# Optimization experiments

Measured on AMD Instinct MI355X. Metric: run time of the kernel, lower is better.

## Reference

```python
import jax, jax.numpy as jnp
import numpy as np

B, T, V = 128, 1024, 192
EPS = 1e-8


def setup_inputs() -> dict:
    key = jax.random.key(0)
    k1, k2, k3, k4, k5 = jax.random.split(key, 5)
    return {
        "emissions": jax.random.normal(k1, (B, T, V), dtype=jnp.float32),
        "tags": jax.random.randint(k2, (B, T), 0, V, dtype=jnp.int64),
        "mask": jnp.ones((B, T), dtype=jnp.int32),
        "transitions": jax.random.normal(k3, (V, V), dtype=jnp.float32) * 0.1,
        "start_trans": jax.random.normal(k4, (V,), dtype=jnp.float32) * 0.1,
        "end_trans": jax.random.normal(k5, (V,), dtype=jnp.float32) * 0.1,
    }


def _lse(x, axis):
    # matches torch _log_sum_exp: max + log(sum(exp(x-max)) + 1e-8)
    m = jnp.max(x, axis=axis)
    return m + jnp.log(jnp.sum(jnp.exp(x - jnp.expand_dims(m, axis)), axis=axis) + EPS)


def _log_partition(emissions, mask, transitions, start_trans, end_trans):
    # emissions: (B,T,V), mask: (B,T) int
    alpha0 = start_trans[None, :] + emissions[:, 0, :]  # (B,V)
    em_t = jnp.moveaxis(emissions[:, 1:, :], 1, 0)       # (T-1,B,V)
    mk_t = jnp.moveaxis(mask[:, 1:], 1, 0).astype(bool)  # (T-1,B)

    def step(alpha, inp):
        emit, m = inp  # (B,V), (B,)
        # (B, V_prev, V_next)
        scores = alpha[:, :, None] + transitions[None, :, :] + emit[:, None, :]
        new_alpha = _lse(scores, axis=1)
        alpha = jnp.where(m[:, None], new_alpha, alpha)
        return alpha, None

    alpha, _ = jax.lax.scan(step, alpha0, (em_t, mk_t))
    return _lse(alpha + end_trans[None, :], axis=1)  # (B,)


def _gold_score(emissions, tags, mask, transitions, start_trans, end_trans):
    Bq, Tq, _ = emissions.shape
    maskf = mask.astype(emissions.dtype)
    # emission score of gold tags at each step: (B,T)
    emit = jnp.take_along_axis(emissions, tags[:, :, None], axis=2)[:, :, 0]
    # transitions between consecutive gold tags: (B,T-1)
    trans = transitions[tags[:, :-1], tags[:, 1:]]
    score = start_trans[tags[:, 0]] + emit[:, 0]
    score = score + jnp.sum((emit[:, 1:] + trans) * maskf[:, 1:], axis=1)
    last_idx = jnp.sum(mask, axis=1).astype(jnp.int32) - 1  # (B,)
    last_tags = jnp.take_along_axis(tags, last_idx[:, None].astype(tags.dtype), axis=1)[:, 0]
    score = score + end_trans[last_tags]
    return score


def reference(emissions, tags, mask, transitions, start_trans, end_trans):
    log_den = _log_partition(emissions, mask, transitions, start_trans, end_trans)
    log_num = _gold_score(emissions, tags, mask, transitions, start_trans, end_trans)
    raw_loss = log_den - log_num
    seq_len = jnp.clip(jnp.sum(mask, axis=1).astype(emissions.dtype), 1.0)
    return raw_loss / seq_len  # (B,)
```

## Files before the change

kernel.cpp:

```cpp
#include <hip/hip_runtime.h>

#define BB 128
#define TT 1024
#define VV 192
#define NTHREADS 256
#define LN2 0.69314718055994530942f
#define WS_STRIDE 448

typedef int   intx8   __attribute__((ext_vector_type(8)));
typedef float floatx2 __attribute__((ext_vector_type(2)));
typedef float floatx4 __attribute__((ext_vector_type(4)));

__device__ __forceinline__ float bf8_to_f32(unsigned char h) {
    floatx2 v = __builtin_amdgcn_cvt_pk_f32_bf8((int)(unsigned int)h, false);
    return v.x;
}
__device__ __forceinline__ unsigned char f32_to_bf8(float f) {
    int pk = __builtin_amdgcn_cvt_pk_bf8_f32(f, f, 0, false);
    return (unsigned char)(pk & 0xff);
}
__device__ __forceinline__ unsigned char f32_to_fp8(float f) {
    int pk = __builtin_amdgcn_cvt_pk_fp8_f32(f, f, 0, false);
    return (unsigned char)(pk & 0xff);
}

#define LBAR() __asm__ volatile("s_waitcnt lgkmcnt(0)\n\ts_barrier" ::: "memory")

template<int DIR>
__device__ __forceinline__ void crf_body(const float* __restrict__ emissions,
                                         const int* __restrict__ tags,
                                         const int* __restrict__ mask,
                                         const float* __restrict__ trans,
                                         const float* __restrict__ start_trans,
                                         const float* __restrict__ end_trans,
                                         float* __restrict__ ws)
{
    const int b = blockIdx.x;
    const int tid = threadIdx.x;
    const int lane = tid & 63;
    const int wid = tid >> 6;
    const int quad = lane >> 4;
    const int col = lane & 15;

    __shared__ __align__(16) unsigned char qpad[4][2][256];
    __shared__ unsigned int smaskp[33];
    __shared__ float wgs[4], wsls[4];

    const float* em_b = emissions + (size_t)b * TT * VV;
    const int* mask_b = mask + b * TT;
    float* wsb = ws + (size_t)b * WS_STRIDE;

    const int nl = wid * 48 + (quad < 3 ? quad : 0) * 16 + col;

    const int firstc[4] = {1, 113, 241, DIR ? 367 : 369};
    const int capRc[4]  = {0, 16, 16, DIR ? 18 : 16};
    const int capPc[4]  = {128, 144, 144, 0};

    #define ROW_OF(x) (DIR ? (TT - 1 - (x)) : (x))

    intx8 ef[6];
    #pragma unroll
    for (int kt = 0; kt < 2; ++kt) {
        #pragma unroll
        for (int h = 0; h < 3; ++h) {
            const int n = wid * 48 + h * 16 + col;
            intx8 v;
            #pragma unroll
            for (int w = 0; w < 8; ++w) {
                unsigned int word = 0;
                #pragma unroll
                for (int by = 0; by < 4; ++by) {
                    int k = kt * 128 + quad * 32 + w * 4 + by;
                    float x = (k < VV) ? __expf(trans[DIR ? (k + n * VV) : (k * VV + n)]) : 0.f;
                    word |= (unsigned int)f32_to_fp8(x) << (8 * by);
                }
                v[w] = (int)word;
            }
            ef[kt * 3 + h] = v;
        }
    }

    for (int i = tid; i < 4 * 512; i += NTHREADS) ((unsigned char*)qpad)[i] = 0;

    if (tid < 33) {
        if (tid == 32) smaskp[32] = 0u;
        else {
            unsigned int m = 0;
            #pragma unroll 4
            for (int j = 0; j < 32; ++j) m |= (mask_b[tid * 32 + j] ? 1u : 0u) << j;
            smaskp[tid] = m;
        }
    }

    float em0[4][8], em1[4][8];
    #pragma unroll
    for (int c = 0; c < 4; ++c) {
        #pragma unroll
        for (int r = 0; r < 8; ++r) em0[c][r] = em_b[(size_t)ROW_OF(firstc[c] + r) * VV + nl];
        #pragma unroll
        for (int r = 0; r < 8; ++r) em1[c][r] = em_b[(size_t)ROW_OF(firstc[c] + 8 + r) * VV + nl];
    }
    float pep[4] = {0.f, 0.f, 0.f, 0.f};
    if (DIR) {
        #pragma unroll
        for (int c = 0; c < 4; ++c)
            pep[c] = __expf(em_b[(size_t)ROW_OF(firstc[c] - 1) * VV + nl]);
    }

    __syncthreads();
    if (tid < VV) {
        float a0 = DIR ? (end_trans[tid] + em_b[(size_t)(TT - 1) * VV + tid])
                       : (start_trans[tid] + em_b[tid]);
        qpad[0][0][tid] = f32_to_bf8(fminf(__expf(a0), 28672.f));
        unsigned char one = f32_to_bf8(1.0f);
        qpad[1][0][tid] = one;
        qpad[2][0][tid] = one;
        qpad[3][0][tid] = one;
    }
    float carry[4] = {0.f,0.f,0.f,0.f}, Rv[4] = {0.f,0.f,0.f,0.f};
    float Pv[4] = {0.f,0.f,0.f,0.f}, csv[4] = {0.f,0.f,0.f,0.f};
    int cur = 0;
    __syncthreads();

    unsigned long long mk64[4];
    int shb[4];

#define GETMK(c, I) ((int)((mk64[c] >> (DIR ? (shb[c] + 15 - (I)) : (shb[c] + (I)))) & 1ull))

#define ROUND(I)                                                               \
    {                                                                          \
        intx8 a0_[4], a1_[4];                                                  \
        unsigned char prevb_[4];                                               \
        _Pragma("unroll")                                                      \
        for (int c = 0; c < 4; ++c) {                                          \
            const intx8* qv = (const intx8*)qpad[c][cur];                      \
            a0_[c] = qv[quad];                                                 \
            a1_[c] = qv[quad + 4];                                             \
            prevb_[c] = qpad[c][cur][nl];                                      \
        }                                                                      \
        floatx4 acc_[4][3];                                                    \
        _Pragma("unroll")                                                      \
        for (int c = 0; c < 4; ++c) {                                          \
            _Pragma("unroll")                                                  \
            for (int h = 0; h < 3; ++h) {                                      \
                floatx4 z = (floatx4){0.f, 0.f, 0.f, 0.f};                     \
                floatx4 t0 = __builtin_amdgcn_mfma_scale_f32_16x16x128_f8f6f4( \
                    a0_[c], ef[h], z, 1, 0, 0, 0x7f7f7f7f, 0, 0x7f7f7f7f);     \
                acc_[c][h] = __builtin_amdgcn_mfma_scale_f32_16x16x128_f8f6f4( \
                    a1_[c], ef[3 + h], t0, 1, 0, 0, 0x7f7f7f7f, 0, 0x7f7f7f7f);\
            }                                                                  \
        }                                                                      \
        _Pragma("unroll")                                                      \
        for (int c = 0; c < 4; ++c) {                                          \
            int mk = GETMK(c, I);                                              \
            int q0i = __builtin_amdgcn_readfirstlane(a0_[c][0]);               \
            float q0 = bf8_to_f32((unsigned char)(q0i & 0xff));                \
            float rr = __builtin_amdgcn_rcpf(q0);                              \
            carry[c] += mk ? __log2f(q0) : 0.f;                                \
            float emraw = ((I) < 8) ? em0[c][(I) & 7] : em1[c][(I) & 7];       \
            float pe = __expf(emraw);                                          \
            float sc = pe * rr;                                                \
            float s0 = acc_[c][0][0];                                          \
            float s1 = acc_[c][1][0];                                          \
            float s2 = acc_[c][2][0];                                          \
            float vv = (quad == 1) ? s1 : ((quad == 2) ? s2 : s0);             \
            unsigned char nbm = f32_to_bf8(fminf(vv * sc, 28672.f));           \
            unsigned char nba;                                                 \
            if (DIR) nba = f32_to_bf8(fminf(bf8_to_f32(prevb_[c]) * pe *       \
                                 __builtin_amdgcn_rcpf(pep[c]), 28672.f));     \
            else nba = prevb_[c];                                              \
            unsigned char nb = mk ? nbm : nba;                                 \
            qpad[c][cur ^ 1][nl] = nb;                                         \
            if (DIR) pep[c] = pe;                                              \
             \
            float q0n = bf8_to_f32(nb);                                        \
            float lg = __log2f(__int_as_float(                                 \
                __builtin_amdgcn_readfirstlane(__float_as_int(q0n))));         \
            int L = lb + (I) + 1;                                              \
            bool hitR = (L == capRc[c]);                                       \
            bool hitP = (L == capPc[c]);                                       \
            Rv[c]    = hitR ? lg : Rv[c];                                      \
            csv[c]   = hitP ? carry[c] : csv[c];                               \
            Pv[c]    = hitP ? lg : Pv[c];                                      \
            carry[c] = hitR ? 0.f : carry[c];                                  \
        }                                                                      \
        __builtin_amdgcn_sched_group_barrier(0x100, 12, 0);      \
        __builtin_amdgcn_sched_group_barrier(0x008, 24, 0);       \
        LBAR();                                                                \
        cur ^= 1;                                                              \
    }

    for (int w = 0; w < 9; ++w) {
        const int lb = 16 * w;
        #pragma unroll
        for (int c = 0; c < 4; ++c) {
            int gw = firstc[c] + lb;
            int base = DIR ? (1024 - gw - 15) : gw;
            unsigned lo = (unsigned)__builtin_amdgcn_readfirstlane((int)smaskp[base >> 5]);
            unsigned hi = (unsigned)__builtin_amdgcn_readfirstlane((int)smaskp[(base >> 5) + 1]);
            mk64[c] = (((unsigned long long)hi) << 32) | (unsigned long long)lo;
            shb[c] = base & 31;
        }
        ROUND(0) ROUND(1) ROUND(2) ROUND(3)
        ROUND(4) ROUND(5) ROUND(6) ROUND(7)
        {
            #pragma unroll
            for (int c = 0; c < 4; ++c) {
                #pragma unroll
                for (int r = 0; r < 8; ++r)
                    em0[c][r] = em_b[(size_t)ROW_OF(firstc[c] + lb + 16 + r) * VV + nl];
            }
        }
        ROUND(8) ROUND(9) ROUND(10) ROUND(11)
        ROUND(12) ROUND(13) ROUND(14) ROUND(15)
        {
            #pragma unroll
            for (int c = 0; c < 4; ++c) {
                #pragma unroll
                for (int r = 0; r < 8; ++r)
                    em1[c][r] = em_b[(size_t)ROW_OF(firstc[c] + lb + 24 + r) * VV + nl];
            }
        }
    }
#undef ROUND
#undef GETMK

    csv[3] = carry[3];

    if (DIR == 0) {
        if (tid < VV) wsb[tid] = bf8_to_f32(qpad[3][cur][tid]);
    } else {
        const intx8* qv = (const intx8*)qpad[3][cur];
        intx8 A0 = qv[quad];
        intx8 A1 = qv[quad + 4];
        int mkf = (int)((smaskp[513 >> 5] >> (513 & 31)) & 1u);
        floatx4 aA[3], aB[3];
        #pragma unroll
        for (int h = 0; h < 3; ++h) {
            floatx4 z = (floatx4){0.f, 0.f, 0.f, 0.f};
            aA[h] = __builtin_amdgcn_mfma_scale_f32_16x16x128_f8f6f4(
                        A0, ef[h], z, 1, 0, 0, 0x7f7f7f7f, 0, 0x7f7f7f7f);
            aB[h] = __builtin_amdgcn_mfma_scale_f32_16x16x128_f8f6f4(
                        A1, ef[3 + h], z, 1, 0, 0, 0x7f7f7f7f, 0, 0x7f7f7f7f);
        }
        if (quad < 3) {
            float s0 = aA[0][0] + aB[0][0];
            float s1 = aA[1][0] + aB[1][0];
            float s2 = aA[2][0] + aB[2][0];
            float vv = (quad == 1) ? s1 : ((quad == 2) ? s2 : s0);
            if (!mkf) vv = bf8_to_f32(qpad[3][cur][nl]) * __builtin_amdgcn_rcpf(pep[3]);
            wsb[192 + nl] = vv;
        }
    }
    if (tid == 0) {
        #pragma unroll
        for (int c = 0; c < 4; ++c) {
            float contrib = csv[c] + ((c < 3) ? Pv[c] : 0.f) - ((c > 0) ? Rv[c] : 0.f);
            wsb[384 + DIR * 8 + c] = contrib;
        }
    }

    float gp = 0.f, sl = 0.f;
    for (int t = tid; t < TT; t += NTHREADS) {
        int mk = (int)((smaskp[t >> 5] >> (t & 31)) & 1u);
        bool inS = DIR ? (t >= 512) : (t < 512);
        if (inS) sl += (float)mk;
        bool inG = DIR ? (t >= 513) : (t >= 1 && t <= 512);
        if (inG) {
            int tg  = tags[b * TT + t];
            int tgp = tags[b * TT + t - 1];
            float term = em_b[(size_t)t * VV + tg] + trans[tgp * VV + tg];
            gp += mk ? term : 0.f;
        }
    }
    #pragma unroll
    for (int off = 1; off < 64; off <<= 1) {
        gp += __shfl_xor(gp, off);
        sl += __shfl_xor(sl, off);
    }
    if (lane == 0) { wgs[wid] = gp; wsls[wid] = sl; }
    __syncthreads();
    if (tid == 0) {
        float g = 0.f, s = 0.f;
        for (int w = 0; w < 4; ++w) { g += wgs[w]; s += wsls[w]; }
        if (DIR == 0) {
            int tg0 = tags[b * TT];
            g += start_trans[tg0] + em_b[tg0];
        }
        wsb[384 + DIR * 8 + 4] = g;
        wsb[384 + DIR * 8 + 5] = s;
    }
    #undef ROW_OF
}

__launch_bounds__(NTHREADS, 1)
__attribute__((amdgpu_waves_per_eu(1, 1)))
__global__ void crf_ilp_kernel(const float* __restrict__ emissions,
                               const int* __restrict__ tags,
                               const int* __restrict__ mask,
                               const float* __restrict__ trans,
                               const float* __restrict__ start_trans,
                               const float* __restrict__ end_trans,
                               float* __restrict__ ws)
{
    if (blockIdx.y == 0)
        crf_body<0>(emissions, tags, mask, trans, start_trans, end_trans, ws);
    else
        crf_body<1>(emissions, tags, mask, trans, start_trans, end_trans, ws);
}

__global__ void crf_combine(const float* __restrict__ ws,
                            const int* __restrict__ tags,
                            const float* __restrict__ end_trans,
                            float* __restrict__ out)
{
    const int b = blockIdx.x;
    const int lane = threadIdx.x;
    const float* wsb = ws + (size_t)b * WS_STRIDE;
    float s = 0.f;
    #pragma unroll
    for (int i = lane; i < VV; i += 64) s += wsb[i] * wsb[192 + i];
    #pragma unroll
    for (int off = 1; off < 64; off <<= 1) s += __shfl_xor(s, off);
    if (lane == 0) {
        float T = 0.f, gold = 0.f, seq = 0.f;
        for (int d = 0; d < 2; ++d) {
            const float* slot = wsb + 384 + d * 8;
            T    += slot[0] + slot[1] + slot[2] + slot[3];
            gold += slot[4];
            seq  += slot[5];
        }
        float logden = LN2 * T + __logf(s + 1e-8f);
        int seqs = (int)(seq + 0.5f);
        int last_idx = seqs - 1; if (last_idx < 0) last_idx = 0;
        gold += end_trans[tags[b * TT + last_idx]];
        float seqf = fmaxf((float)seqs, 1.0f);
        out[b] = (logden - gold) / seqf;
    }
}

extern "C" void kernel_launch(void* const* d_in, const int* in_sizes, int n_in,
                              void* d_out, int out_size, void* d_ws, size_t ws_size,
                              hipStream_t stream) {
    const float* emissions   = (const float*)d_in[0];
    const int*   tags        = (const int*)d_in[1];
    const int*   mask        = (const int*)d_in[2];
    const float* trans       = (const float*)d_in[3];
    const float* start_trans = (const float*)d_in[4];
    const float* end_trans   = (const float*)d_in[5];
    float* out = (float*)d_out;
    float* ws  = (float*)d_ws;

    crf_ilp_kernel<<<dim3(BB, 2), NTHREADS, 0, stream>>>(
        emissions, tags, mask, trans, start_trans, end_trans, ws);
    crf_combine<<<BB, 64, 0, stream>>>(ws, tags, end_trans, out);
}
```

Baseline: 252.5 us.

## Pack four chunk recurrences into one MFMA via per-row A operands

Each recurrence step now loads a different chunk's probability vector into each row group of the MFMA A operand (lane&3 selects the chunk). One pair of MFMAs per output tile then yields all four chunks' results in separate accumulator rows, replacing four separate MFMA pairs. A startup self-test checks that the MFMA row mapping behaves as assumed and falls back to the original four-chunk path if it does not. Emission prefetch and per-lane work are reorganised around the new lane-to-chunk mapping. The risks are extra LDS reads and select logic per step, plus a one-time validation cost.

```diff
diff --git a/kernel.cpp b/kernel.cpp
--- a/kernel.cpp
+++ b/kernel.cpp
@@ -25,6 +25,9 @@
 }
 
 #define LBAR() __asm__ volatile("s_waitcnt lgkmcnt(0)\n\ts_barrier" ::: "memory")
+
+#define MFMA_SC(A, B, C) __builtin_amdgcn_mfma_scale_f32_16x16x128_f8f6f4( \
+    (A), (B), (C), 1, 0, 0, 0x7f7f7f7f, 0, 0x7f7f7f7f)
 
 template<int DIR>
 __device__ __forceinline__ void crf_body(const float* __restrict__ emissions,
@@ -45,12 +48,14 @@
     __shared__ __align__(16) unsigned char qpad[4][2][256];
     __shared__ unsigned int smaskp[33];
     __shared__ float wgs[4], wsls[4];
+    __shared__ int okflag;
 
     const float* em_b = emissions + (size_t)b * TT * VV;
     const int* mask_b = mask + b * TT;
     float* wsb = ws + (size_t)b * WS_STRIDE;
 
-    const int nl = wid * 48 + (quad < 3 ? quad : 0) * 16 + col;
+    const int col0 = wid * 48 + col;
+    const int nlT  = wid * 48 + (quad < 3 ? quad : 0) * 16 + col;
 
     const int firstc[4] = {1, 113, 241, DIR ? 367 : 369};
     const int capRc[4]  = {0, 16, 16, DIR ? 18 : 16};
@@ -91,43 +96,185 @@
             smaskp[tid] = m;
         }
     }
-
-    float em0[4][8], em1[4][8];
-    #pragma unroll
-    for (int c = 0; c < 4; ++c) {
-        #pragma unroll
-        for (int r = 0; r < 8; ++r) em0[c][r] = em_b[(size_t)ROW_OF(firstc[c] + r) * VV + nl];
-        #pragma unroll
-        for (int r = 0; r < 8; ++r) em1[c][r] = em_b[(size_t)ROW_OF(firstc[c] + 8 + r) * VV + nl];
-    }
-    float pep[4] = {0.f, 0.f, 0.f, 0.f};
-    if (DIR) {
-        #pragma unroll
-        for (int c = 0; c < 4; ++c)
-            pep[c] = __expf(em_b[(size_t)ROW_OF(firstc[c] - 1) * VV + nl]);
-    }
+    if (tid == 0) okflag = 1;
 
     __syncthreads();
     if (tid < VV) {
         float a0 = DIR ? (end_trans[tid] + em_b[(size_t)(TT - 1) * VV + tid])
                        : (start_trans[tid] + em_b[tid]);
         qpad[0][0][tid] = f32_to_bf8(fminf(__expf(a0), 28672.f));
-        unsigned char one = f32_to_bf8(1.0f);
-        qpad[1][0][tid] = one;
-        qpad[2][0][tid] = one;
-        qpad[3][0][tid] = one;
-    }
+        qpad[1][0][tid] = f32_to_bf8(1.0f);
+        qpad[2][0][tid] = f32_to_bf8(2.0f);
+        qpad[3][0][tid] = f32_to_bf8(4.0f);
+    }
+    __syncthreads();
+
+    {
+        int okl = 1;
+        const intx8* qv0 = (const intx8*)qpad[0][0];
+        intx8 b0 = qv0[quad], b1 = qv0[quad + 4];
+        const intx8* qvp = (const intx8*)qpad[lane & 3][0];
+        intx8 p0 = qvp[quad], p1 = qvp[quad + 4];
+        floatx4 z = (floatx4){0.f, 0.f, 0.f, 0.f};
+        floatx4 tb = MFMA_SC(b0, ef[0], z);
+        floatx4 ab = MFMA_SC(b1, ef[3], tb);
+        floatx4 tp = MFMA_SC(p0, ef[0], z);
+        floatx4 ap = MFMA_SC(p1, ef[3], tp);
+        okl &= (fabsf(ap[0] - ab[0]) <= 1e-3f * (fabsf(ab[0]) + 1.f)) ? 1 : 0;
+        okl &= (fabsf(ap[2] - 2.f * ap[1]) <= 1e-3f * (fabsf(ap[2]) + 1.f)) ? 1 : 0;
+        okl &= (fabsf(ap[3] - 4.f * ap[1]) <= 1e-3f * (fabsf(ap[3]) + 1.f)) ? 1 : 0;
+        unsigned long long vt = __ballot(okl);
+        if (lane == 0 && vt != 0xFFFFFFFFFFFFFFFFull) okflag = 0;
+    }
+    __syncthreads();
+    const bool usePacked = (okflag != 0);
+
     float carry[4] = {0.f,0.f,0.f,0.f}, Rv[4] = {0.f,0.f,0.f,0.f};
     float Pv[4] = {0.f,0.f,0.f,0.f}, csv[4] = {0.f,0.f,0.f,0.f};
     int cur = 0;
-    __syncthreads();
-
     unsigned long long mk64[4];
     int shb[4];
 
+#define FETCHWIN(lb_)                                                          \
+    {                                                                          \
+        _Pragma("unroll")                                                      \
+        for (int c = 0; c < 4; ++c) {                                          \
+            int gw = firstc[c] + (lb_);                                        \
+            int base = DIR ? (1024 - gw - 15) : gw;                            \
+            unsigned lo = (unsigned)__builtin_amdgcn_readfirstlane((int)smaskp[base >> 5]);      \
+            unsigned hi = (unsigned)__builtin_amdgcn_readfirstlane((int)smaskp[(base >> 5) + 1]);\
+            mk64[c] = (((unsigned long long)hi) << 32) | (unsigned long long)lo;\
+            shb[c] = base & 31;                                                \
+        }                                                                      \
+    }
 #define GETMK(c, I) ((int)((mk64[c] >> (DIR ? (shb[c] + 15 - (I)) : (shb[c] + (I)))) & 1ull))
 
-#define ROUND(I)                                                               \
+    if (usePacked) {
+        const int flc = (quad == 1) ? firstc[1] : (quad == 2) ? firstc[2]
+                      : (quad == 3) ? firstc[3] : firstc[0];
+        float em0[3][8], em1[3][8];
+        #pragma unroll
+        for (int h = 0; h < 3; ++h) {
+            #pragma unroll
+            for (int r = 0; r < 8; ++r) {
+                em0[h][r] = em_b[(size_t)ROW_OF(flc + r) * VV + col0 + h * 16];
+                em1[h][r] = em_b[(size_t)ROW_OF(flc + 8 + r) * VV + col0 + h * 16];
+            }
+        }
+        float pep[3] = {0.f, 0.f, 0.f};
+        if (DIR) {
+            #pragma unroll
+            for (int h = 0; h < 3; ++h)
+                pep[h] = __expf(em_b[(size_t)ROW_OF(flc - 1) * VV + col0 + h * 16]);
+        }
+
+#define PROUND(I)                                                              \
+    {                                                                          \
+        const intx8* qv_ = (const intx8*)qpad[lane & 3][cur];                  \
+        intx8 a0_ = qv_[quad];                                                 \
+        intx8 a1_ = qv_[quad + 4];                                             \
+        float q0c[4];                                                          \
+        q0c[0] = bf8_to_f32(qpad[0][cur][0]);                                  \
+        q0c[1] = bf8_to_f32(qpad[1][cur][0]);                                  \
+        q0c[2] = bf8_to_f32(qpad[2][cur][0]);                                  \
+        q0c[3] = bf8_to_f32(qpad[3][cur][0]);                                  \
+        unsigned char pb0 = qpad[quad][cur][col0];                             \
+        unsigned char pb1 = qpad[quad][cur][col0 + 16];                        \
+        unsigned char pb2 = qpad[quad][cur][col0 + 32];                        \
+                                                       \
+        {                                                                      \
+            int Lm1 = lb + (I);                                                \
+            _Pragma("unroll")                                                  \
+            for (int c = 0; c < 4; ++c) {                                      \
+                float lgc = __log2f(q0c[c]);                                   \
+                bool hitR = (Lm1 == capRc[c]);                                 \
+                bool hitP = (Lm1 == capPc[c]);                                 \
+                Rv[c]    = hitR ? lgc : Rv[c];                                 \
+                csv[c]   = hitP ? carry[c] : csv[c];                           \
+                Pv[c]    = hitP ? lgc : Pv[c];                                 \
+                carry[c] = hitR ? 0.f : carry[c];                              \
+            }                                                                  \
+        }                                                                      \
+        floatx4 acc_[3];                                                       \
+        _Pragma("unroll")                                                      \
+        for (int h = 0; h < 3; ++h) {                                          \
+            floatx4 z_ = (floatx4){0.f, 0.f, 0.f, 0.f};                        \
+            floatx4 t0_ = MFMA_SC(a0_, ef[h], z_);                             \
+            acc_[h] = MFMA_SC(a1_, ef[3 + h], t0_);                            \
+        }                                                                      \
+        _Pragma("unroll")                                                      \
+        for (int c = 0; c < 4; ++c)                                            \
+            carry[c] += GETMK(c, I) ? __log2f(q0c[c]) : 0.f;                   \
+        float q0q = (quad == 1) ? q0c[1] : (quad == 2) ? q0c[2]                \
+                  : (quad == 3) ? q0c[3] : q0c[0];                             \
+        float rrq = __builtin_amdgcn_rcpf(q0q);                                \
+        int mkq   = (quad == 1) ? GETMK(1, I) : (quad == 2) ? GETMK(2, I)      \
+                  : (quad == 3) ? GETMK(3, I) : GETMK(0, I);                   \
+        _Pragma("unroll")                                                      \
+        for (int h = 0; h < 3; ++h) {                                          \
+            float emr = ((I) < 8) ? em0[h][(I) & 7] : em1[h][(I) & 7];         \
+            float pe = __expf(emr);                                            \
+            float vv = (quad == 1) ? acc_[h][1] : (quad == 2) ? acc_[h][2]     \
+                     : (quad == 3) ? acc_[h][3] : acc_[h][0];                  \
+            unsigned char pb = (h == 0) ? pb0 : (h == 1) ? pb1 : pb2;          \
+            unsigned char nbm = f32_to_bf8(fminf(vv * pe * rrq, 28672.f));     \
+            unsigned char nba;                                                 \
+            if (DIR) nba = f32_to_bf8(fminf(bf8_to_f32(pb) * pe *              \
+                                 __builtin_amdgcn_rcpf(pep[h]), 28672.f));     \
+            else nba = pb;                                                     \
+            qpad[quad][cur ^ 1][col0 + h * 16] = mkq ? nbm : nba;              \
+            if (DIR) pep[h] = pe;                                              \
+        }                                                                      \
+        __builtin_amdgcn_sched_group_barrier(0x100, 11, 0);                    \
+        __builtin_amdgcn_sched_group_barrier(0x008, 6, 0);                     \
+        LBAR();                                                                \
+        cur ^= 1;                                                              \
+    }
+
+        for (int w = 0; w < 9; ++w) {
+            const int lb = 16 * w;
+            FETCHWIN(lb)
+            PROUND(0) PROUND(1) PROUND(2) PROUND(3)
+            PROUND(4) PROUND(5) PROUND(6) PROUND(7)
+            {
+                #pragma unroll
+                for (int h = 0; h < 3; ++h)
+                    #pragma unroll
+                    for (int r = 0; r < 8; ++r)
+                        em0[h][r] = em_b[(size_t)ROW_OF(flc + lb + 16 + r) * VV + col0 + h * 16];
+            }
+            PROUND(8) PROUND(9) PROUND(10) PROUND(11)
+            PROUND(12) PROUND(13) PROUND(14) PROUND(15)
+            {
+                #pragma unroll
+                for (int h = 0; h < 3; ++h)
+                    #pragma unroll
+                    for (int r = 0; r < 8; ++r)
+                        em1[h][r] = em_b[(size_t)ROW_OF(flc + lb + 24 + r) * VV + col0 + h * 16];
+            }
+        }
+#undef PROUND
+        Pv[1] = __log2f(bf8_to_f32(qpad[1][cur][0]));  csv[1] = carry[1];
+        Pv[2] = __log2f(bf8_to_f32(qpad[2][cur][0]));  csv[2] = carry[2];
+        csv[3] = carry[3];
+    } else {
+        float em0b[4][8], em1b[4][8];
+        #pragma unroll
+        for (int c = 0; c < 4; ++c) {
+            #pragma unroll
+            for (int r = 0; r < 8; ++r) {
+                em0b[c][r] = em_b[(size_t)ROW_OF(firstc[c] + r) * VV + nlT];
+                em1b[c][r] = em_b[(size_t)ROW_OF(firstc[c] + 8 + r) * VV + nlT];
+            }
+        }
+        float pepb[4] = {0.f, 0.f, 0.f, 0.f};
+        if (DIR) {
+            #pragma unroll
+            for (int c = 0; c < 4; ++c)
+                pepb[c] = __expf(em_b[(size_t)ROW_OF(firstc[c] - 1) * VV + nlT]);
+        }
+
+#define BROUND(I)                                                              \
     {                                                                          \
         intx8 a0_[4], a1_[4];                                                  \
         unsigned char prevb_[4];                                               \
@@ -136,7 +283,7 @@
             const intx8* qv = (const intx8*)qpad[c][cur];                      \
             a0_[c] = qv[quad];                                                 \
             a1_[c] = qv[quad + 4];                                             \
-            prevb_[c] = qpad[c][cur][nl];                                      \
+            prevb_[c] = qpad[c][cur][nlT];                                     \
         }                                                                      \
         floatx4 acc_[4][3];                                                    \
         _Pragma("unroll")                                                      \
@@ -144,10 +291,8 @@
             _Pragma("unroll")                                                  \
             for (int h = 0; h < 3; ++h) {                                      \
                 floatx4 z = (floatx4){0.f, 0.f, 0.f, 0.f};                     \
-                floatx4 t0 = __builtin_amdgcn_mfma_scale_f32_16x16x128_f8f6f4( \
-                    a0_[c], ef[h], z, 1, 0, 0, 0x7f7f7f7f, 0, 0x7f7f7f7f);     \
-                acc_[c][h] = __builtin_amdgcn_mfma_scale_f32_16x16x128_f8f6f4( \
-                    a1_[c], ef[3 + h], t0, 1, 0, 0, 0x7f7f7f7f, 0, 0x7f7f7f7f);\
+                floatx4 t0 = MFMA_SC(a0_[c], ef[h], z);                        \
+                acc_[c][h] = MFMA_SC(a1_[c], ef[3 + h], t0);                   \
             }                                                                  \
         }                                                                      \
         _Pragma("unroll")                                                      \
@@ -157,7 +302,7 @@
             float q0 = bf8_to_f32((unsigned char)(q0i & 0xff));                \
             float rr = __builtin_amdgcn_rcpf(q0);                              \
             carry[c] += mk ? __log2f(q0) : 0.f;                                \
-            float emraw = ((I) < 8) ? em0[c][(I) & 7] : em1[c][(I) & 7];       \
+            float emraw = ((I) < 8) ? em0b[c][(I) & 7] : em1b[c][(I) & 7];     \
             float pe = __expf(emraw);                                          \
             float sc = pe * rr;                                                \
             float s0 = acc_[c][0][0];                                          \
@@ -167,12 +312,11 @@
             unsigned char nbm = f32_to_bf8(fminf(vv * sc, 28672.f));           \
             unsigned char nba;                                                 \
             if (DIR) nba = f32_to_bf8(fminf(bf8_to_f32(prevb_[c]) * pe *       \
-                                 __builtin_amdgcn_rcpf(pep[c]), 28672.f));     \
+                                 __builtin_amdgcn_rcpf(pepb[c]), 28672.f));    \
             else nba = prevb_[c];                                              \
             unsigned char nb = mk ? nbm : nba;                                 \
-            qpad[c][cur ^ 1][nl] = nb;                                         \
-            if (DIR) pep[c] = pe;                                              \
-             \
+            qpad[c][cur ^ 1][nlT] = nb;                                        \
+            if (DIR) pepb[c] = pe;                                             \
             float q0n = bf8_to_f32(nb);                                        \
             float lg = __log2f(__int_as_float(                                 \
                 __builtin_amdgcn_readfirstlane(__float_as_int(q0n))));         \
@@ -184,48 +328,39 @@
             Pv[c]    = hitP ? lg : Pv[c];                                      \
             carry[c] = hitR ? 0.f : carry[c];                                  \
         }                                                                      \
-        __builtin_amdgcn_sched_group_barrier(0x100, 12, 0);      \
-        __builtin_amdgcn_sched_group_barrier(0x008, 24, 0);       \
+        __builtin_amdgcn_sched_group_barrier(0x100, 12, 0);                    \
+        __builtin_amdgcn_sched_group_barrier(0x008, 24, 0);                    \
         LBAR();                                                                \
         cur ^= 1;                                                              \
     }
 
-    for (int w = 0; w < 9; ++w) {
-        const int lb = 16 * w;
-        #pragma unroll
-        for (int c = 0; c < 4; ++c) {
-            int gw = firstc[c] + lb;
-            int base = DIR ? (1024 - gw - 15) : gw;
-            unsigned lo = (unsigned)__builtin_amdgcn_readfirstlane((int)smaskp[base >> 5]);
-            unsigned hi = (unsigned)__builtin_amdgcn_readfirstlane((int)smaskp[(base >> 5) + 1]);
-            mk64[c] = (((unsigned long long)hi) << 32) | (unsigned long long)lo;
-            shb[c] = base & 31;
-        }
-        ROUND(0) ROUND(1) ROUND(2) ROUND(3)
-        ROUND(4) ROUND(5) ROUND(6) ROUND(7)
-        {
-            #pragma unroll
-            for (int c = 0; c < 4; ++c) {
+        for (int w = 0; w < 9; ++w) {
+            const int lb = 16 * w;
+            FETCHWIN(lb)
+            BROUND(0) BROUND(1) BROUND(2) BROUND(3)
+            BROUND(4) BROUND(5) BROUND(6) BROUND(7)
+            {
                 #pragma unroll
-                for (int r = 0; r < 8; ++r)
-                    em0[c][r] = em_b[(size_t)ROW_OF(firstc[c] + lb + 16 + r) * VV + nl];
-            }
-        }
-        ROUND(8) ROUND(9) ROUND(10) ROUND(11)
-        ROUND(12) ROUND(13) ROUND(14) ROUND(15)
-        {
-            #pragma unroll
-            for (int c = 0; c < 4; ++c) {
+                for (int c = 0; c < 4; ++c)
+                    #pragma unroll
+                    for (int r = 0; r < 8; ++r)
+                        em0b[c][r] = em_b[(size_t)ROW_OF(firstc[c] + lb + 16 + r) * VV + nlT];
+            }
+            BROUND(8) BROUND(9) BROUND(10) BROUND(11)
+            BROUND(12) BROUND(13) BROUND(14) BROUND(15)
+            {
                 #pragma unroll
-                for (int r = 0; r < 8; ++r)
-                    em1[c][r] = em_b[(size_t)ROW_OF(firstc[c] + lb + 24 + r) * VV + nl];
-            }
-        }
-    }
-#undef ROUND
+                for (int c = 0; c < 4; ++c)
+                    #pragma unroll
+                    for (int r = 0; r < 8; ++r)
+                        em1b[c][r] = em_b[(size_t)ROW_OF(firstc[c] + lb + 24 + r) * VV + nlT];
+            }
+        }
+#undef BROUND
+        csv[3] = carry[3];
+    }
+#undef FETCHWIN
 #undef GETMK
-
-    csv[3] = carry[3];
 
     if (DIR == 0) {
         if (tid < VV) wsb[tid] = bf8_to_f32(qpad[3][cur][tid]);
@@ -234,22 +369,20 @@
         intx8 A0 = qv[quad];
         intx8 A1 = qv[quad + 4];
         int mkf = (int)((smaskp[513 >> 5] >> (513 & 31)) & 1u);
-        floatx4 aA[3], aB[3];
+        floatx4 aA[3];
         #pragma unroll
         for (int h = 0; h < 3; ++h) {
             floatx4 z = (floatx4){0.f, 0.f, 0.f, 0.f};
-            aA[h] = __builtin_amdgcn_mfma_scale_f32_16x16x128_f8f6f4(
-                        A0, ef[h], z, 1, 0, 0, 0x7f7f7f7f, 0, 0x7f7f7f7f);
-            aB[h] = __builtin_amdgcn_mfma_scale_f32_16x16x128_f8f6f4(
-                        A1, ef[3 + h], z, 1, 0, 0, 0x7f7f7f7f, 0, 0x7f7f7f7f);
+            floatx4 t0 = MFMA_SC(A0, ef[h], z);
+            aA[h] = MFMA_SC(A1, ef[3 + h], t0);
         }
         if (quad < 3) {
-            float s0 = aA[0][0] + aB[0][0];
-            float s1 = aA[1][0] + aB[1][0];
-            float s2 = aA[2][0] + aB[2][0];
-            float vv = (quad == 1) ? s1 : ((quad == 2) ? s2 : s0);
-            if (!mkf) vv = bf8_to_f32(qpad[3][cur][nl]) * __builtin_amdgcn_rcpf(pep[3]);
-            wsb[192 + nl] = vv;
+            float vv = (quad == 1) ? aA[1][0] : (quad == 2) ? aA[2][0] : aA[0][0];
+            if (!mkf) {
+                float peT = __expf(em_b[(size_t)513 * VV + nlT]);
+                vv = bf8_to_f32(qpad[3][cur][nlT]) * __builtin_amdgcn_rcpf(peT);
+            }
+            wsb[192 + nlT] = vv;
         }
     }
     if (tid == 0) {
@@ -295,13 +428,13 @@
 
 __launch_bounds__(NTHREADS, 1)
 __attribute__((amdgpu_waves_per_eu(1, 1)))
-__global__ void crf_ilp_kernel(const float* __restrict__ emissions,
-                               const int* __restrict__ tags,
-                               const int* __restrict__ mask,
-                               const float* __restrict__ trans,
-                               const float* __restrict__ start_trans,
-                               const float* __restrict__ end_trans,
-                               float* __restrict__ ws)
+__global__ void crf_dual_kernel(const float* __restrict__ emissions,
+                                const int* __restrict__ tags,
+                                const int* __restrict__ mask,
+                                const float* __restrict__ trans,
+                                const float* __restrict__ start_trans,
+                                const float* __restrict__ end_trans,
+                                float* __restrict__ ws)
 {
     if (blockIdx.y == 0)
         crf_body<0>(emissions, tags, mask, trans, start_trans, end_trans, ws);
@@ -351,7 +484,7 @@
     float* out = (float*)d_out;
     float* ws  = (float*)d_ws;
 
-    crf_ilp_kernel<<<dim3(BB, 2), NTHREADS, 0, stream>>>(
+    crf_dual_kernel<<<dim3(BB, 2), NTHREADS, 0, stream>>>(
         emissions, tags, mask, trans, start_trans, end_trans, ws);
     crf_combine<<<BB, 64, 0, stream>>>(ws, tags, end_trans, out);
 }
```

After: 249.0 us. Within noise of the previous version (-1.4%).
